# Kernel optimization log

Hardware: AMD Instinct MI355X
Metric: run time of the kernel (lower is better)

## Reference

```python
import jax, jax.numpy as jnp
import numpy as np

DT = 0.001        # norse default integration step
ALPHA = 100.0     # norse SuperSpike surrogate-gradient sharpness
V_LEAK = 0.0
V_RESET = 0.0

@jax.custom_vjp
def superspike(x):
    # Heaviside forward, SuperSpike surrogate backward (norse default 'super')
    return (x > 0).astype(x.dtype)

def _ss_fwd(x):
    return superspike(x), x

def _ss_bwd(x, g):
    return (g / (ALPHA * jnp.abs(x) + 1.0) ** 2,)

superspike.defvjp(_ss_fwd, _ss_bwd)

def lif_box_scan(x_tbf, tau, vth):
    # x_tbf: [T,B,F]; tau, vth: [3,1,1] (one per LIF population)
    # norse LIFBox: v' = v + dt*tau_mem_inv*(v_leak - v + i); z = H(v'-v_th); v = (1-z)*v' + z*v_reset
    T, B, F = x_tbf.shape
    v0 = jnp.zeros((3, B, F), x_tbf.dtype)
    def step(v, x):
        v_dec = v + DT * tau * (V_LEAK - v + x)   # broadcasts x [B,F] -> [3,B,F]
        z = superspike(v_dec - vth)
        v_new = (1.0 - z) * v_dec + z * V_RESET
        return v_new, z
    _, zs = jax.lax.scan(step, v0, x_tbf)
    return zs  # [T,3,B,F]

def setup_inputs() -> dict:
    key = jax.random.key(0)
    ks = jax.random.split(key, 10)
    B, F, T = 64, 26, 8192
    inputs = jax.random.uniform(ks[0], (B, F, T), dtype=jnp.float32)
    tau = jnp.array([200.0, 300.0, 600.0], dtype=jnp.float32)
    vth = jnp.array([0.006, 0.008, 0.013], dtype=jnp.float32)
    # Conv2d(3->1, 1x1): weight [1,3,1,1] -> store as [3], bias [1]
    conv_w = jax.random.normal(ks[1], (3,), dtype=jnp.float32) * (1.0 / np.sqrt(3.0))
    conv_b = jax.random.normal(ks[2], (1,), dtype=jnp.float32) * 0.1
    w1 = jax.random.normal(ks[3], (12, 26), dtype=jnp.float32) * (1.0 / np.sqrt(26.0))
    b1 = jax.random.normal(ks[4], (12,), dtype=jnp.float32) * 0.1
    w2 = jax.random.normal(ks[5], (4, 12), dtype=jnp.float32) * (1.0 / np.sqrt(12.0))
    b2 = jax.random.normal(ks[6], (4,), dtype=jnp.float32) * 0.1
    w3 = jax.random.normal(ks[7], (2, 4), dtype=jnp.float32) * (1.0 / np.sqrt(4.0))
    b3 = jax.random.normal(ks[8], (2,), dtype=jnp.float32) * 0.1
    return {"inputs": inputs, "tau": tau, "vth": vth, "conv_w": conv_w,
            "conv_b": conv_b, "w1": w1, "b1": b1, "w2": w2, "b2": b2,
            "w3": w3, "b3": b3}

def reference(inputs, tau, vth, conv_w, conv_b, w1, b1, w2, b2, w3, b3):
    # inputs: [B, 26, T]
    x = jnp.transpose(inputs, (2, 0, 1))                     # [T,B,F]
    zs = lif_box_scan(x, tau[:, None, None], vth[:, None, None])  # [T,3,B,F]
    # 1x1 conv over the 3 population channels (no spatial mixing)
    h = jnp.einsum('tcbf,c->btf', zs, conv_w) + conv_b[0]    # [B,T,F]
    h = h @ w1.T + b1                                        # [B,T,12]
    h = h @ w2.T + b2                                        # [B,T,4]
    h = h @ w3.T + b3                                        # [B,T,2]
    return jnp.transpose(h, (0, 2, 1))                       # [B,2,T]
```

## Files before the change

### kernel.cpp

```cpp
#include <hip/hip_runtime.h>

#define T_TOTAL 8192
#define NB      64
#define NF      26
#define NCHAIN  78
#define NCH_P   80
#define TCS     64
#define CPB     4
#define TB      256
#define CHUNKS  2
#define WARM    8
#define NSCAN   (NCHAIN * CPB)
#define BLOCK   320
#define ROWW    (TB + WARM)
#define RSTRIDE 266
#define ZROW    84

__device__ __forceinline__ unsigned lif_step(float& v, float a, float th, float x) {
    float t1 = x - v;
    float vd = __fadd_rn(v, __fmul_rn(a, t1));
    unsigned z = (vd > th) ? 1u : 0u;
    v = z ? 0.0f : vd;
    return z;
}

__global__ __launch_bounds__(BLOCK, 5)
void snn_fused_kernel(const float* __restrict__ x,
                      const float* __restrict__ tau,
                      const float* __restrict__ vth,
                      const float* __restrict__ conv_w,
                      const float* __restrict__ conv_b,
                      const float* __restrict__ w1,
                      const float* __restrict__ b1,
                      const float* __restrict__ w2,
                      const float* __restrict__ b2,
                      const float* __restrict__ w3,
                      const float* __restrict__ b3,
                      float* __restrict__ out)
{
    const int blk = blockIdx.x;
    const int b   = blockIdx.y;
    const int tid = threadIdx.x;

    __shared__ __align__(16) float    sX[NF * RSTRIDE];
    __shared__ __align__(16) unsigned sZ[2 * CPB * ZROW];
    __shared__ __align__(16) float    sC0[NCH_P];
    __shared__ __align__(16) float    sC1[NCH_P];
    __shared__ float sMr[2][NF];
    __shared__ float sConst[2];

    const float* xb = x + (size_t)b * NF * T_TOTAL;

    if (tid < NCHAIN) {
        const int c = tid / NF, f = tid % NF;
        float m0 = 0.0f, m1 = 0.0f;
        #pragma unroll
        for (int j = 0; j < 4; ++j) {
            float a = 0.0f;
            #pragma unroll
            for (int k = 0; k < 12; ++k) a += w2[j * 12 + k] * w1[k * NF + f];
            m0 += w3[j] * a;
            m1 += w3[4 + j] * a;
        }
        const float cw = conv_w[c];
        sC0[tid] = m0 * cw;
        sC1[tid] = m1 * cw;
        if (c == 0) { sMr[0][f] = m0; sMr[1][f] = m1; }
    } else if (tid < NCH_P) {
        sC0[tid] = 0.0f;
        sC1[tid] = 0.0f;
    }

    const int ch = (tid < NSCAN) ? tid % NCHAIN : 0;
    const int k  = (tid < NSCAN) ? tid / NCHAIN : 0;
    const int c_ = ch / NF, f_ = ch % NF;
    const float a_ = __fmul_rn(0.001f, tau[c_]);
    const float th = vth[c_];

    const int wrd  = tid >> 4;
    const int bit0 = (tid & 15) * 2;

    auto stage = [&](int tb, int lo, int nthr) {
        if (tid < lo) return;
        for (int i = tid - lo; i < NF * (ROWW / 4); i += nthr) {
            const int f = i / (ROWW / 4);
            const int q = i - f * (ROWW / 4);
            int t4 = tb - WARM + 4 * q;
            t4 = (t4 < 0) ? 0 : t4;
            const float4 xv = *(const float4*)(xb + (size_t)f * T_TOTAL + t4);
            float* dst = sX + f * RSTRIDE + 4 * q;
            *(float2*)(dst + 0) = make_float2(xv.x, xv.y);
            *(float2*)(dst + 2) = make_float2(xv.z, xv.w);
        }
    };

    auto scan = [&](bool nowarm) {
        const float* row = sX + f_ * RSTRIDE;
        const int j0 = WARM + k * TCS;
        float v = 0.0f;
        if (!nowarm) {
            const float2* rw = (const float2*)(row + j0 - WARM);
            #pragma unroll
            for (int q = 0; q < WARM / 2; ++q) {
                float2 xv = rw[q];
                lif_step(v, a_, th, xv.x);
                lif_step(v, a_, th, xv.y);
            }
        }
        const float2* rm = (const float2*)(row + j0);
        #pragma unroll
        for (int w = 0; w < 2; ++w) {
            unsigned bw = 0;
            #pragma unroll
            for (int q = 0; q < 16; ++q) {
                float2 xv = rm[w * 16 + q];
                bw |= lif_step(v, a_, th, xv.x) << (2 * q);
                bw |= lif_step(v, a_, th, xv.y) << (2 * q + 1);
            }
            sZ[(2 * k + w) * ZROW + ch] = bw;
        }
    };

    auto reduce = [&](int tb) {
        float acc0[2], acc1[2];
        const float k0 = sConst[0], k1 = sConst[1];
        acc0[0] = acc0[1] = k0;
        acc1[0] = acc1[1] = k1;
        #pragma unroll 4
        for (int g = 0; g < NCH_P / 4; ++g) {
            const uint4  zw = *(const uint4*)(sZ + wrd * ZROW + 4 * g);
            const float4 c0 = *(const float4*)(sC0 + 4 * g);
            const float4 c1 = *(const float4*)(sC1 + 4 * g);
            const unsigned zz[4] = {zw.x, zw.y, zw.z, zw.w};
            const float cc0[4] = {c0.x, c0.y, c0.z, c0.w};
            const float cc1[4] = {c1.x, c1.y, c1.z, c1.w};
            #pragma unroll
            for (int i = 0; i < 4; ++i) {
                #pragma unroll
                for (int j = 0; j < 2; ++j) {
                    const float s = (float)((zz[i] >> (bit0 + j)) & 1u);
                    acc0[j] = fmaf(s, cc0[i], acc0[j]);
                    acc1[j] = fmaf(s, cc1[i], acc1[j]);
                }
            }
        }
        const size_t t = (size_t)tb + (size_t)tid * 2;
        *(float2*)(out + ((size_t)b * 2 + 0) * T_TOTAL + t) = make_float2(acc0[0], acc0[1]);
        *(float2*)(out + ((size_t)b * 2 + 1) * T_TOTAL + t) = make_float2(acc1[0], acc1[1]);
    };

    const int tb0 = blk * (CHUNKS * TB);
    const int tb1 = tb0 + TB;

    stage(tb0, 0, BLOCK);
    __syncthreads();

    if (tid < NSCAN) {
        scan(blk == 0 && k == 0);
    } else if (tid == NSCAN) {
        float ab[4];
        #pragma unroll
        for (int j = 0; j < 4; ++j) {
            float a = b2[j];
            #pragma unroll
            for (int kk = 0; kk < 12; ++kk) a += w2[j * 12 + kk] * b1[kk];
            ab[j] = a;
        }
        #pragma unroll
        for (int o = 0; o < 2; ++o) {
            float s = b3[o];
            #pragma unroll
            for (int j = 0; j < 4; ++j) s += w3[o * 4 + j] * ab[j];
            float msum = 0.0f;
            for (int f = 0; f < NF; ++f) msum += sMr[o][f];
            sConst[o] = s + conv_b[0] * msum;
        }
    }
    __syncthreads();

    if (tid < 128) reduce(tb0);
    stage(tb1, 128, BLOCK - 128);
    __syncthreads();

    if (tid < NSCAN) scan(false);
    __syncthreads();

    if (tid < 128) reduce(tb1);
}

extern "C" void kernel_launch(void* const* d_in, const int* in_sizes, int n_in,
                              void* d_out, int out_size, void* d_ws, size_t ws_size,
                              hipStream_t stream) {
    const float* x      = (const float*)d_in[0];
    const float* tau    = (const float*)d_in[1];
    const float* vth    = (const float*)d_in[2];
    const float* conv_w = (const float*)d_in[3];
    const float* conv_b = (const float*)d_in[4];
    const float* w1     = (const float*)d_in[5];
    const float* b1     = (const float*)d_in[6];
    const float* w2     = (const float*)d_in[7];
    const float* b2     = (const float*)d_in[8];
    const float* w3     = (const float*)d_in[9];
    const float* b3     = (const float*)d_in[10];
    float* out = (float*)d_out;

    dim3 grid(T_TOTAL / (CHUNKS * TB), NB);
    snn_fused_kernel<<<grid, BLOCK, 0, stream>>>(x, tau, vth, conv_w, conv_b,
                                                 w1, b1, w2, b2, w3, b3, out);
}
```

Measured before the change: 114.1 us.

## Double-buffer input tiles with async global-to-LDS loads over four chunks

Replaces the register-staged global-to-shared copy with direct global_load_lds 16-byte transfers into a double-buffered shared tile. Each block now processes four 256-step chunks, prefetching the next chunk while the current one is scanned. The reduce stage is widened to one output per thread over 256 threads, and scan reads use float4. This aims to hide global load latency behind the serial LIF scans, at the cost of doubled LDS, fewer blocks per CU (launch bounds lowered to 2) and half as many blocks in the grid.

```diff
diff --git a/kernel.cpp b/kernel.cpp
--- a/kernel.cpp
+++ b/kernel.cpp
@@ -8,12 +8,16 @@
 #define TCS     64
 #define CPB     4
 #define TB      256
-#define CHUNKS  2
+#define CHUNKS  4
 #define WARM    8
 #define NSCAN   (NCHAIN * CPB)
 #define BLOCK   320
-#define ROWW    (TB + WARM)
-#define RSTRIDE 266
+#define NWAVE   (BLOCK / 64)
+#define RSTRIDE 268
+#define QROW    (RSTRIDE / 4)
+#define NQPAD   1792
+#define NLOADI  (NQPAD / 64)
+#define SXF     (NQPAD * 4)
 #define ZROW    84
 
 __device__ __forceinline__ unsigned lif_step(float& v, float a, float th, float x) {
@@ -24,7 +28,13 @@
     return z;
 }
 
-__global__ __launch_bounds__(BLOCK, 5)
+__device__ __forceinline__ void gload16(const float* g, float* l) {
+    __builtin_amdgcn_global_load_lds(
+        (const __attribute__((address_space(1))) void*)g,
+        (__attribute__((address_space(3))) void*)l, 16, 0, 0);
+}
+
+__global__ __launch_bounds__(BLOCK, 2)
 void snn_fused_kernel(const float* __restrict__ x,
                       const float* __restrict__ tau,
                       const float* __restrict__ vth,
@@ -42,7 +52,7 @@
     const int b   = blockIdx.y;
     const int tid = threadIdx.x;
 
-    __shared__ __align__(16) float    sX[NF * RSTRIDE];
+    __shared__ __align__(16) float    sX[2][SXF];
     __shared__ __align__(16) unsigned sZ[2 * CPB * ZROW];
     __shared__ __align__(16) float    sC0[NCH_P];
     __shared__ __align__(16) float    sC1[NCH_P];
@@ -58,7 +68,7 @@
         for (int j = 0; j < 4; ++j) {
             float a = 0.0f;
             #pragma unroll
-            for (int k = 0; k < 12; ++k) a += w2[j * 12 + k] * w1[k * NF + f];
+            for (int kk = 0; kk < 12; ++kk) a += w2[j * 12 + kk] * w1[kk * NF + f];
             m0 += w3[j] * a;
             m1 += w3[4 + j] * a;
         }
@@ -71,64 +81,61 @@
         sC1[tid] = 0.0f;
     }
 
+    const int wave = tid >> 6, lane = tid & 63;
+
     const int ch = (tid < NSCAN) ? tid % NCHAIN : 0;
     const int k  = (tid < NSCAN) ? tid / NCHAIN : 0;
     const int c_ = ch / NF, f_ = ch % NF;
     const float a_ = __fmul_rn(0.001f, tau[c_]);
     const float th = vth[c_];
 
-    const int wrd  = tid >> 4;
-    const int bit0 = (tid & 15) * 2;
-
-    auto stage = [&](int tb, int lo, int nthr) {
-        if (tid < lo) return;
-        for (int i = tid - lo; i < NF * (ROWW / 4); i += nthr) {
-            const int f = i / (ROWW / 4);
-            const int q = i - f * (ROWW / 4);
+    auto prefetch = [&](int buf, int tb) {
+        for (int i = wave; i < NLOADI; i += NWAVE) {
+            const int Q = i * 64 + lane;
+            int f = Q / QROW;
+            int q = Q - f * QROW;
             int t4 = tb - WARM + 4 * q;
-            t4 = (t4 < 0) ? 0 : t4;
-            const float4 xv = *(const float4*)(xb + (size_t)f * T_TOTAL + t4);
-            float* dst = sX + f * RSTRIDE + 4 * q;
-            *(float2*)(dst + 0) = make_float2(xv.x, xv.y);
-            *(float2*)(dst + 2) = make_float2(xv.z, xv.w);
+            if (f >= NF || q >= QROW - 1) { f = 0; t4 = 0; }
+            if (t4 < 0) t4 = 0;
+            gload16(xb + (size_t)f * T_TOTAL + t4, &sX[buf][i * 256]);
         }
     };
 
-    auto scan = [&](bool nowarm) {
-        const float* row = sX + f_ * RSTRIDE;
+    auto scan = [&](int buf, bool nowarm) {
+        const float* row = &sX[buf][f_ * RSTRIDE];
         const int j0 = WARM + k * TCS;
         float v = 0.0f;
         if (!nowarm) {
-            const float2* rw = (const float2*)(row + j0 - WARM);
-            #pragma unroll
-            for (int q = 0; q < WARM / 2; ++q) {
-                float2 xv = rw[q];
-                lif_step(v, a_, th, xv.x);
-                lif_step(v, a_, th, xv.y);
-            }
-        }
-        const float2* rm = (const float2*)(row + j0);
+            const float4 wa = *(const float4*)(row + j0 - WARM);
+            const float4 wb = *(const float4*)(row + j0 - WARM + 4);
+            lif_step(v, a_, th, wa.x); lif_step(v, a_, th, wa.y);
+            lif_step(v, a_, th, wa.z); lif_step(v, a_, th, wa.w);
+            lif_step(v, a_, th, wb.x); lif_step(v, a_, th, wb.y);
+            lif_step(v, a_, th, wb.z); lif_step(v, a_, th, wb.w);
+        }
+        const float4* rm = (const float4*)(row + j0);
         #pragma unroll
         for (int w = 0; w < 2; ++w) {
             unsigned bw = 0;
             #pragma unroll
-            for (int q = 0; q < 16; ++q) {
-                float2 xv = rm[w * 16 + q];
-                bw |= lif_step(v, a_, th, xv.x) << (2 * q);
-                bw |= lif_step(v, a_, th, xv.y) << (2 * q + 1);
+            for (int q = 0; q < 8; ++q) {
+                float4 xv = rm[w * 8 + q];
+                bw |= lif_step(v, a_, th, xv.x) << (4 * q);
+                bw |= lif_step(v, a_, th, xv.y) << (4 * q + 1);
+                bw |= lif_step(v, a_, th, xv.z) << (4 * q + 2);
+                bw |= lif_step(v, a_, th, xv.w) << (4 * q + 3);
             }
             sZ[(2 * k + w) * ZROW + ch] = bw;
         }
     };
 
     auto reduce = [&](int tb) {
-        float acc0[2], acc1[2];
-        const float k0 = sConst[0], k1 = sConst[1];
-        acc0[0] = acc0[1] = k0;
-        acc1[0] = acc1[1] = k1;
+        const int r = tid >> 5, bit = tid & 31;
+        float acc0 = sConst[0], acc1 = sConst[1];
+        const unsigned* zr = sZ + r * ZROW;
         #pragma unroll 4
         for (int g = 0; g < NCH_P / 4; ++g) {
-            const uint4  zw = *(const uint4*)(sZ + wrd * ZROW + 4 * g);
+            const uint4  zw = *(const uint4*)(zr + 4 * g);
             const float4 c0 = *(const float4*)(sC0 + 4 * g);
             const float4 c1 = *(const float4*)(sC1 + 4 * g);
             const unsigned zz[4] = {zw.x, zw.y, zw.z, zw.w};
@@ -136,56 +143,55 @@
             const float cc1[4] = {c1.x, c1.y, c1.z, c1.w};
             #pragma unroll
             for (int i = 0; i < 4; ++i) {
+                const float s = (float)((zz[i] >> bit) & 1u);
+                acc0 = fmaf(s, cc0[i], acc0);
+                acc1 = fmaf(s, cc1[i], acc1);
+            }
+        }
+        const size_t t = (size_t)tb + tid;
+        out[((size_t)b * 2 + 0) * T_TOTAL + t] = acc0;
+        out[((size_t)b * 2 + 1) * T_TOTAL + t] = acc1;
+    };
+
+    const int tb0 = blk * (CHUNKS * TB);
+
+    prefetch(0, tb0);
+    __syncthreads();
+
+    int cur = 0;
+    for (int cc = 0; cc < CHUNKS; ++cc) {
+        const int tb = tb0 + cc * TB;
+
+        if (cc + 1 < CHUNKS) prefetch(cur ^ 1, tb + TB);
+
+        if (tid < NSCAN) {
+            scan(cur, blk == 0 && cc == 0 && k == 0);
+        } else if (tid == NSCAN && cc == 0) {
+            float ab[4];
+            #pragma unroll
+            for (int j = 0; j < 4; ++j) {
+                float a = b2[j];
                 #pragma unroll
-                for (int j = 0; j < 2; ++j) {
-                    const float s = (float)((zz[i] >> (bit0 + j)) & 1u);
-                    acc0[j] = fmaf(s, cc0[i], acc0[j]);
-                    acc1[j] = fmaf(s, cc1[i], acc1[j]);
-                }
-            }
-        }
-        const size_t t = (size_t)tb + (size_t)tid * 2;
-        *(float2*)(out + ((size_t)b * 2 + 0) * T_TOTAL + t) = make_float2(acc0[0], acc0[1]);
-        *(float2*)(out + ((size_t)b * 2 + 1) * T_TOTAL + t) = make_float2(acc1[0], acc1[1]);
-    };
-
-    const int tb0 = blk * (CHUNKS * TB);
-    const int tb1 = tb0 + TB;
-
-    stage(tb0, 0, BLOCK);
-    __syncthreads();
-
-    if (tid < NSCAN) {
-        scan(blk == 0 && k == 0);
-    } else if (tid == NSCAN) {
-        float ab[4];
-        #pragma unroll
-        for (int j = 0; j < 4; ++j) {
-            float a = b2[j];
-            #pragma unroll
-            for (int kk = 0; kk < 12; ++kk) a += w2[j * 12 + kk] * b1[kk];
-            ab[j] = a;
-        }
-        #pragma unroll
-        for (int o = 0; o < 2; ++o) {
-            float s = b3[o];
-            #pragma unroll
-            for (int j = 0; j < 4; ++j) s += w3[o * 4 + j] * ab[j];
-            float msum = 0.0f;
-            for (int f = 0; f < NF; ++f) msum += sMr[o][f];
-            sConst[o] = s + conv_b[0] * msum;
-        }
+                for (int kk = 0; kk < 12; ++kk) a += w2[j * 12 + kk] * b1[kk];
+                ab[j] = a;
+            }
+            #pragma unroll
+            for (int o = 0; o < 2; ++o) {
+                float s = b3[o];
+                #pragma unroll
+                for (int j = 0; j < 4; ++j) s += w3[o * 4 + j] * ab[j];
+                float msum = 0.0f;
+                for (int f = 0; f < NF; ++f) msum += sMr[o][f];
+                sConst[o] = s + conv_b[0] * msum;
+            }
+        }
+        __syncthreads();
+
+        if (tid < TB) reduce(tb);
+        __syncthreads();
+
+        cur ^= 1;
     }
-    __syncthreads();
-
-    if (tid < 128) reduce(tb0);
-    stage(tb1, 128, BLOCK - 128);
-    __syncthreads();
-
-    if (tid < NSCAN) scan(false);
-    __syncthreads();
-
-    if (tid < 128) reduce(tb1);
 }
 
 extern "C" void kernel_launch(void* const* d_in, const int* in_sizes, int n_in,
```

Result: slower. 125.2 us (+9.7%).
